# Kernel optimization log

Hardware: AMD Instinct MI355X
Metric: run time of the kernel (lower is better)

The kernel has to match this reference:

```python
import jax, jax.numpy as jnp
import numpy as np

NUM_HEADS = 8
D_MODEL = 512
HEAD_DIM = D_MODEL // NUM_HEADS


def _conv1x1(x, W, b):
    # Conv1d(kernel_size=1): x [B, Cin, N], W [Cout, Cin], b [Cout] -> [B, Cout, N]
    return jnp.einsum('oi,bin->bon', W, x) + b[None, :, None]


def setup_inputs() -> dict:
    key = jax.random.key(0)
    ks = jax.random.split(key, 12)
    B, D, N, Mlen = 4, D_MODEL, 2048, 2048
    inp = {
        'query': jax.random.normal(ks[0], (B, D, N), dtype=jnp.float32),
        'key':   jax.random.normal(ks[1], (B, D, Mlen), dtype=jnp.float32),
        'value': jax.random.normal(ks[2], (B, D, Mlen), dtype=jnp.float32),
        'M':     jnp.ones((B, N, Mlen), dtype=jnp.int32),
    }
    scale = 0.02
    inp['Wq'] = jax.random.normal(ks[3], (D, D), dtype=jnp.float32) * scale
    inp['bq'] = jnp.zeros((D,), dtype=jnp.float32)
    inp['Wk'] = jax.random.normal(ks[4], (D, D), dtype=jnp.float32) * scale
    inp['bk'] = jnp.zeros((D,), dtype=jnp.float32)
    inp['Wv'] = jax.random.normal(ks[5], (D, D), dtype=jnp.float32) * scale
    inp['bv'] = jnp.zeros((D,), dtype=jnp.float32)
    inp['Wm'] = jax.random.normal(ks[6], (D, D), dtype=jnp.float32) * scale
    inp['bm'] = jnp.zeros((D,), dtype=jnp.float32)
    return inp


def reference(query, key, value, M, Wq, bq, Wk, bk, Wv, bv, Wm, bm):
    B = query.shape[0]
    # 1x1-conv projections, then channel split as [head_dim, heads] (matches torch .view)
    q = _conv1x1(query, Wq, bq).reshape(B, HEAD_DIM, NUM_HEADS, -1)  # [B, d, h, N]
    k = _conv1x1(key,   Wk, bk).reshape(B, HEAD_DIM, NUM_HEADS, -1)  # [B, d, h, M]
    v = _conv1x1(value, Wv, bv).reshape(B, HEAD_DIM, NUM_HEADS, -1)  # [B, d, h, M]
    scores = jnp.einsum('bdhn,bdhm->bhnm', q, k) / jnp.sqrt(jnp.float32(HEAD_DIM))
    # mask: positions with M==0 are disallowed -> fill with -finfo.max
    bad = (1 - M)[:, None, :, :].astype(bool)  # [B, 1, N, M], broadcasts over heads
    scores = jnp.where(bad, -jnp.finfo(scores.dtype).max, scores)
    prob = jax.nn.softmax(scores, axis=-1)  # [B, h, N, M]
    x = jnp.einsum('bhnm,bdhm->bdhn', prob, v)  # [B, d, h, N]
    out = _conv1x1(x.reshape(B, HEAD_DIM * NUM_HEADS, -1), Wm, bm)  # [B, D, N]
    return out
```

## Files before the change

### kernel.cpp

```cpp
#include <hip/hip_runtime.h>

typedef __attribute__((ext_vector_type(8))) short s8v;
typedef __attribute__((ext_vector_type(4))) float f4v;
typedef unsigned short u16;
typedef unsigned long long u64;

#define DM 512
#define NH 8
#define HD 64
#define BB 4
#define NN 2048

__device__ __forceinline__ float bf2f(u16 x){ return __uint_as_float(((unsigned)x)<<16); }
__device__ __forceinline__ u16 f2bf(float f){
  unsigned u = __float_as_uint(f);
  u += 0x7FFFu + ((u>>16)&1u);
  return (u16)(u>>16);
}

__global__ void k_permute(const float* Wq, const float* bq, const float* Wk, const float* bk,
                          const float* Wv, const float* bv, const float* Wm,
                          u16* Wp, u16* Wmp, float* bp){
  int blk = blockIdx.x, tid = threadIdx.x;
  if (blk < 1536){
    int t = blk >> 9, op = blk & 511;
    int srow = ((op & 63) << 3) | (op >> 6);
    const float* W = (t==0) ? Wq : ((t==1) ? Wk : Wv);
    for (int j = tid; j < 512; j += 256)
      Wp[((size_t)t*512 + op)*512 + j] = f2bf(W[(size_t)srow*512 + j]);
  } else if (blk < 2048){
    int o = blk - 1536;
    for (int c = tid; c < 512; c += 256){
      int scol = ((c & 63) << 3) | (c >> 6);
      Wmp[(size_t)o*512 + c] = f2bf(Wm[(size_t)o*512 + scol]);
    }
  } else {
    for (int idx = tid; idx < 1536; idx += 256){
      int t = idx >> 9, op = idx & 511;
      const float* bs = (t==0) ? bq : ((t==1) ? bk : bv);
      int srow = ((op & 63) << 3) | (op >> 6);
      bp[idx] = bs[srow];
    }
  }
}

__global__ __launch_bounds__(256) void k_transpose(const float* q, const float* k, const float* v, u16* XT){
  __shared__ u16 T[64*72];
  int blk = blockIdx.x, tid = threadIdx.x;
  int rt = blk & 31; blk >>= 5;
  int it = blk & 7;  blk >>= 3;
  int b  = blk & 3;  int t = blk >> 2;
  const float* src = (t==0) ? q : ((t==1) ? k : v);
  src += (size_t)b*DM*NN;
  int i0 = it*64, r0 = rt*64;
  int il = tid>>4, rj = (tid&15)*4;
  #pragma unroll
  for (int p=0;p<4;p++){
    int i = il + p*16;
    float4 vv = *(const float4*)&src[(size_t)(i0+i)*NN + r0 + rj];
    float fv[4] = {vv.x, vv.y, vv.z, vv.w};
    #pragma unroll
    for (int qq=0;qq<4;qq++){
      int r = rj + qq;
      int sr = ((r&3)<<4) | (r>>2);
      T[sr*72 + i] = f2bf(fv[qq]);
    }
  }
  __syncthreads();
  u16* dst = XT + ((size_t)(t*4+b)*NN)*DM;
  int rl = tid>>3, ib = (tid&7)*8;
  #pragma unroll
  for (int p=0;p<2;p++){
    int r = rl + p*32;
    int sr = ((r&3)<<4) | (r>>2);
    s8v vv = *(s8v*)&T[sr*72 + ib];
    *(s8v*)&dst[(size_t)(r0+r)*DM + i0 + ib] = vv;
  }
}

__global__ __launch_bounds__(256) void k_proj(const u16* XT, const u16* Wp, const float* bp,
                                              u16* P, u16* VT){
  __shared__ u16 Xl[64*40];
  __shared__ u16 Wl[64*40];
  __shared__ u16 S[64*66];
  int blk = blockIdx.x, tid = threadIdx.x;
  int ot = blk & 7;  blk >>= 3;
  int rt = blk & 31; blk >>= 5;
  int b  = blk & 3;  int t = blk >> 2;
  int r0 = rt*64, o0 = ot*64;
  const u16* Xbase = XT + ((size_t)(t*4+b)*NN + r0)*DM;
  const u16* Wbase = Wp + ((size_t)t*512 + o0)*DM;
  int lr = tid>>2, lk = (tid&3)*8;
  int w = tid>>6, L = tid&63, li = L&15, lq = L>>4;
  f4v acc[4];
  #pragma unroll
  for (int j=0;j<4;j++) acc[j] = (f4v){0.f,0.f,0.f,0.f};
  for (int kk=0; kk<16; kk++){
    int k0 = kk*32;
    __syncthreads();
    *(s8v*)&Xl[lr*40+lk] = *(const s8v*)&Xbase[(size_t)lr*DM + k0 + lk];
    *(s8v*)&Wl[lr*40+lk] = *(const s8v*)&Wbase[(size_t)lr*DM + k0 + lk];
    __syncthreads();
    s8v a = *(s8v*)&Xl[(w*16+li)*40 + lq*8];
    #pragma unroll
    for (int j=0;j<4;j++){
      s8v bf = *(s8v*)&Wl[(j*16+li)*40 + lq*8];
      acc[j] = __builtin_amdgcn_mfma_f32_16x16x32_bf16(a, bf, acc[j], 0, 0, 0);
    }
  }
  int h = o0 >> 6;
  if (t < 2){
    float scale = (t==0) ? 0.125f : 1.0f;
    u16* Pb = P + (((size_t)(t*4+b)*NH + h)*NN)*HD;
    #pragma unroll
    for (int j=0;j<4;j++){
      int col = j*16 + li;
      float bias = bp[t*512 + o0 + col];
      #pragma unroll
      for (int ri=0; ri<4; ri++){
        int row = r0 + w*16 + lq*4 + ri;
        Pb[(size_t)row*HD + col] = f2bf((acc[j][ri] + bias)*scale);
      }
    }
  } else {
    #pragma unroll
    for (int j=0;j<4;j++){
      int col = j*16 + li;
      float bias = bp[2*512 + o0 + col];
      #pragma unroll
      for (int ri=0; ri<4; ri++){
        int rloc = w*16 + lq*4 + ri;
        S[rloc*66 + col] = f2bf(acc[j][ri] + bias);
      }
    }
    __syncthreads();
    int dl = tid>>2;
    u16* Vb = VT + (((size_t)b*NH + h)*HD)*NN;
    #pragma unroll
    for (int c=0;c<2;c++){
      int moff = (tid&3)*8 + c*32;
      s8v vv; u16* vp = (u16*)&vv;
      #pragma unroll
      for (int jj=0;jj<8;jj++) vp[jj] = S[(moff+jj)*66 + dl];
      *(s8v*)&Vb[(size_t)dl*NN + r0 + moff] = vv;
    }
  }
}

__global__ void k_maskpack(const int* M, u64* bits){
  int tid = threadIdx.x;
  size_t word = (size_t)blockIdx.x*4 + (tid>>6);
  int lane = tid & 63;
  int v = M[word*64 + lane];
  u64 bal = __ballot(v == 1);
  if (lane == 0) bits[word] = bal;
}

__global__ __launch_bounds__(256) void k_flash(const u16* P, const u16* VT, const u64* bits, u16* Xout){
  __shared__ u16 Ql[64*72];
  __shared__ u16 Kl[64*72];
  __shared__ u16 Vt[64*72];
  __shared__ u16 Pl[64*72];
  int blk = blockIdx.x, tid = threadIdx.x;
  int nt = blk & 31; int bh = blk >> 5;
  int b = bh >> 3, h = bh & 7;
  int n0 = nt*64;
  const size_t TSZ = (size_t)BB*NH*NN*HD;
  const u16* Qb = P + ((size_t)bh*NN + n0)*HD;
  const u16* Kb = P + TSZ + (size_t)bh*NN*HD;
  const u16* Vb = VT + (size_t)bh*HD*NN;

  int sm = tid>>3, sd = (tid&7)*8;
  int w = tid>>6, L = tid&63, li = L&15, lq = L>>4;
  int sli = ((li&3)<<2) | (li>>2);

  #pragma unroll
  for (int p=0;p<2;p++)
    *(s8v*)&Ql[(sm+p*32)*72 + sd] = *(const s8v*)&Qb[(size_t)(sm+p*32)*HD + sd];

  float ls[4];
  f4v O[4];
  #pragma unroll
  for (int ri=0;ri<4;ri++) ls[ri] = 0.f;
  #pragma unroll
  for (int j=0;j<4;j++) O[j] = (f4v){0.f,0.f,0.f,0.f};

  for (int mt=0; mt<32; mt++){
    int m0 = mt*64;
    s8v kreg[2], vreg[2];
    #pragma unroll
    for (int p=0;p<2;p++){
      kreg[p] = *(const s8v*)&Kb[(size_t)(m0+sm+p*32)*HD + sd];
      vreg[p] = *(const s8v*)&Vb[(size_t)(sm+p*32)*NN + m0 + sd];
    }
    u64 mw[4];
    #pragma unroll
    for (int ri=0;ri<4;ri++)
      mw[ri] = bits[((size_t)b*NN + n0 + w*16 + lq*4 + ri)*32 + mt];

    __syncthreads();
    #pragma unroll
    for (int p=0;p<2;p++){
      *(s8v*)&Kl[(sm+p*32)*72 + sd] = kreg[p];
      *(s8v*)&Vt[(sm+p*32)*72 + sd] = vreg[p];
    }
    __syncthreads();

    s8v a0 = *(s8v*)&Ql[(w*16+li)*72 + lq*8];
    s8v a1 = *(s8v*)&Ql[(w*16+li)*72 + 32 + lq*8];
    f4v S[4];
    #pragma unroll
    for (int j=0;j<4;j++){
      s8v b0 = *(s8v*)&Kl[(j*16+li)*72 + lq*8];
      s8v b1 = *(s8v*)&Kl[(j*16+li)*72 + 32 + lq*8];
      f4v c = (f4v){0.f,0.f,0.f,0.f};
      c = __builtin_amdgcn_mfma_f32_16x16x32_bf16(a0, b0, c, 0, 0, 0);
      c = __builtin_amdgcn_mfma_f32_16x16x32_bf16(a1, b1, c, 0, 0, 0);
      S[j] = c;
    }

    #pragma unroll
    for (int ri=0;ri<4;ri++){
      u64 wd = mw[ri];
      int srow = (w*16 + ((ri&3)<<2) + lq)*72;
      #pragma unroll
      for (int j=0;j<4;j++){
        float e = __expf(S[j][ri]);
        e = ((wd>>(j*16+li)) & 1ull) ? e : 0.f;
        ls[ri] += e;
        Pl[srow + j*16 + li] = f2bf(e);
      }
    }

    s8v ap0 = *(s8v*)&Pl[(w*16+sli)*72 + lq*8];
    s8v ap1 = *(s8v*)&Pl[(w*16+sli)*72 + 32 + lq*8];
    #pragma unroll
    for (int j2=0;j2<4;j2++){
      s8v b0 = *(s8v*)&Vt[(j2*16+li)*72 + lq*8];
      s8v b1 = *(s8v*)&Vt[(j2*16+li)*72 + 32 + lq*8];
      O[j2] = __builtin_amdgcn_mfma_f32_16x16x32_bf16(ap0, b0, O[j2], 0, 0, 0);
      O[j2] = __builtin_amdgcn_mfma_f32_16x16x32_bf16(ap1, b1, O[j2], 0, 0, 0);
    }
  }

  #pragma unroll
  for (int ri=0;ri<4;ri++){
    float r = ls[ri];
    r += __shfl_xor(r,1,16); r += __shfl_xor(r,2,16);
    r += __shfl_xor(r,4,16); r += __shfl_xor(r,8,16);
    ls[ri] = (r > 0.f) ? 1.0f/r : 0.f;
  }
  u16* Xo = Xout + ((size_t)b*NN)*DM + h*HD;
  #pragma unroll
  for (int j2=0;j2<4;j2++){
    int d = j2*16 + li;
    #pragma unroll
    for (int ri=0;ri<4;ri++){
      int n = n0 + w*16 + lq*4 + ri;
      Xo[(size_t)n*DM + d] = f2bf(O[j2][ri]*ls[ri]);
    }
  }
}

__global__ __launch_bounds__(256) void k_out(const u16* Wmp, const u16* Xout, const float* bm, float* out){
  __shared__ u16 Wl[64*40];
  __shared__ u16 Xl[64*40];
  int blk = blockIdx.x, tid = threadIdx.x;
  int nt = blk & 31; blk >>= 5;
  int ot = blk & 7;  int b = blk >> 3;
  int o0 = ot*64, n0 = nt*64;
  int lr = tid>>2, lk = (tid&3)*8;
  int w = tid>>6, L = tid&63, li = L&15, lq = L>>4;
  f4v acc[4];
  #pragma unroll
  for (int j=0;j<4;j++) acc[j] = (f4v){0.f,0.f,0.f,0.f};
  for (int kk=0; kk<16; kk++){
    int k0 = kk*32;
    __syncthreads();
    *(s8v*)&Wl[lr*40+lk] = *(const s8v*)&Wmp[(size_t)(o0+lr)*DM + k0 + lk];
    *(s8v*)&Xl[lr*40+lk] = *(const s8v*)&Xout[((size_t)b*NN + n0+lr)*DM + k0 + lk];
    __syncthreads();
    s8v a = *(s8v*)&Wl[(w*16+li)*40 + lq*8];
    #pragma unroll
    for (int j=0;j<4;j++){
      s8v bf = *(s8v*)&Xl[(j*16+li)*40 + lq*8];
      acc[j] = __builtin_amdgcn_mfma_f32_16x16x32_bf16(a, bf, acc[j], 0, 0, 0);
    }
  }
  #pragma unroll
  for (int j=0;j<4;j++){
    int n = n0 + j*16 + li;
    #pragma unroll
    for (int ri=0;ri<4;ri++){
      int o = o0 + w*16 + lq*4 + ri;
      out[((size_t)b*DM + o)*NN + n] = acc[j][ri] + bm[o];
    }
  }
}

extern "C" void kernel_launch(void* const* d_in, const int* in_sizes, int n_in,
                              void* d_out, int out_size, void* d_ws, size_t ws_size,
                              hipStream_t stream){
  const float* q  = (const float*)d_in[0];
  const float* k  = (const float*)d_in[1];
  const float* v  = (const float*)d_in[2];
  const int*   M  = (const int*)d_in[3];
  const float* Wq = (const float*)d_in[4];
  const float* bq = (const float*)d_in[5];
  const float* Wk = (const float*)d_in[6];
  const float* bk = (const float*)d_in[7];
  const float* Wv = (const float*)d_in[8];
  const float* bv = (const float*)d_in[9];
  const float* Wm = (const float*)d_in[10];
  const float* bm = (const float*)d_in[11];

  char* ws = (char*)d_ws;
  u16*   XT   = (u16*)(ws + 0);
  u16*   P    = (u16*)(ws + 25165824);
  u16*   VT   = (u16*)(ws + 41943040);
  u16*   Wp   = (u16*)(ws + 50331648);
  u16*   Wmp  = (u16*)(ws + 51904512);
  float* bp   = (float*)(ws + 52428800);
  u64*   bits = (u64*)(ws + 52434944);
  u16*   Xout = (u16*)(ws + 54532096);
  float* out  = (float*)d_out;

  k_permute<<<2049, 256, 0, stream>>>(Wq, bq, Wk, bk, Wv, bv, Wm, Wp, Wmp, bp);
  k_transpose<<<3072, 256, 0, stream>>>(q, k, v, XT);
  k_proj<<<3072, 256, 0, stream>>>(XT, Wp, bp, P, VT);
  k_maskpack<<<65536, 256, 0, stream>>>(M, bits);
  k_flash<<<1024, 256, 0, stream>>>(P, VT, bits, Xout);
  k_out<<<1024, 256, 0, stream>>>(Wmp, Xout, bm, out);
}
```

Before: 316.5 us.

## Use 128x128 GEMM tiles with direct-to-LDS loads, add mask-skip fast path and MFMA row sums

The projection and output GEMMs move from 64x64 to 128x128 block tiles with 4x4 MFMA accumulators per wave. Operands are loaded through global_load_lds into an XOR-swizzled LDS layout, which cuts block count and raises operand reuse. A new kernel ANDs mask bits per 64x64 tile so flash attention can skip per-row mask loads and selects when a tile is fully unmasked. Softmax row sums are now computed with an extra MFMA against a ones vector instead of shuffle reductions. This adds register pressure and an extra tiny kernel launch, and the row sums are now taken from bf16-rounded probabilities.

```diff
diff --git a/kernel.cpp b/kernel.cpp
--- a/kernel.cpp
+++ b/kernel.cpp
@@ -16,6 +16,10 @@
   unsigned u = __float_as_uint(f);
   u += 0x7FFFu + ((u>>16)&1u);
   return (u16)(u>>16);
+}
+__device__ __forceinline__ void gl2lds16(const u16* g, u16* l){
+  __builtin_amdgcn_global_load_lds((__attribute__((address_space(1))) void*)(g),
+                                   (__attribute__((address_space(3))) void*)(l), 16, 0, 0);
 }
 
 __global__ void k_permute(const float* Wq, const float* bq, const float* Wk, const float* bk,
@@ -80,69 +84,102 @@
 
 __global__ __launch_bounds__(256) void k_proj(const u16* XT, const u16* Wp, const float* bp,
                                               u16* P, u16* VT){
-  __shared__ u16 Xl[64*40];
-  __shared__ u16 Wl[64*40];
-  __shared__ u16 S[64*66];
+  __shared__ u16 Al[128*32];
+  __shared__ u16 Bl[128*32];
+  __shared__ u16 S[128*72];
   int blk = blockIdx.x, tid = threadIdx.x;
-  int ot = blk & 7;  blk >>= 3;
-  int rt = blk & 31; blk >>= 5;
-  int b  = blk & 3;  int t = blk >> 2;
-  int r0 = rt*64, o0 = ot*64;
-  const u16* Xbase = XT + ((size_t)(t*4+b)*NN + r0)*DM;
-  const u16* Wbase = Wp + ((size_t)t*512 + o0)*DM;
-  int lr = tid>>2, lk = (tid&3)*8;
+  int nt = blk & 3; int mt = blk >> 2;
+  int tb = mt >> 4;
+  int t  = tb >> 2, b = tb & 3;
+  int r0 = (mt & 15)*128, o0 = nt*128;
+  const u16* Abase = XT + ((size_t)tb*NN + r0)*DM;
+  const u16* Bbase = Wp + ((size_t)t*512 + o0)*DM;
+
   int w = tid>>6, L = tid&63, li = L&15, lq = L>>4;
-  f4v acc[4];
-  #pragma unroll
-  for (int j=0;j<4;j++) acc[j] = (f4v){0.f,0.f,0.f,0.f};
+  int wr = w>>1, wc = w&1;
+  int srow = tid>>2;
+  int g8   = ((tid&3) ^ ((tid>>3)&3))*8;
+  u16* AldsW = &Al[((tid&192))*8];
+  u16* BldsW = &Bl[((tid&192))*8];
+  int sw = (li>>1)&3;
+
+  f4v acc[4][4];
+  #pragma unroll
+  for (int a=0;a<4;a++)
+    #pragma unroll
+    for (int c2=0;c2<4;c2++) acc[a][c2] = (f4v){0.f,0.f,0.f,0.f};
+
   for (int kk=0; kk<16; kk++){
     int k0 = kk*32;
     __syncthreads();
-    *(s8v*)&Xl[lr*40+lk] = *(const s8v*)&Xbase[(size_t)lr*DM + k0 + lk];
-    *(s8v*)&Wl[lr*40+lk] = *(const s8v*)&Wbase[(size_t)lr*DM + k0 + lk];
-    __syncthreads();
-    s8v a = *(s8v*)&Xl[(w*16+li)*40 + lq*8];
-    #pragma unroll
-    for (int j=0;j<4;j++){
-      s8v bf = *(s8v*)&Wl[(j*16+li)*40 + lq*8];
-      acc[j] = __builtin_amdgcn_mfma_f32_16x16x32_bf16(a, bf, acc[j], 0, 0, 0);
-    }
-  }
-  int h = o0 >> 6;
+    #pragma unroll
+    for (int c=0;c<2;c++){
+      gl2lds16(&Abase[(size_t)(srow + c*64)*DM + k0 + g8], AldsW + c*2048);
+      gl2lds16(&Bbase[(size_t)(srow + c*64)*DM + k0 + g8], BldsW + c*2048);
+    }
+    __syncthreads();
+    s8v af[4], bfr[4];
+    #pragma unroll
+    for (int a=0;a<4;a++){
+      int r = wr*64 + a*16 + li;
+      af[a] = *(s8v*)&Al[r*32 + ((lq ^ sw))*8];
+    }
+    #pragma unroll
+    for (int c2=0;c2<4;c2++){
+      int r = wc*64 + c2*16 + li;
+      bfr[c2] = *(s8v*)&Bl[r*32 + ((lq ^ sw))*8];
+    }
+    #pragma unroll
+    for (int a=0;a<4;a++)
+      #pragma unroll
+      for (int c2=0;c2<4;c2++)
+        acc[a][c2] = __builtin_amdgcn_mfma_f32_16x16x32_bf16(af[a], bfr[c2], acc[a][c2], 0, 0, 0);
+  }
+
   if (t < 2){
     float scale = (t==0) ? 0.125f : 1.0f;
-    u16* Pb = P + (((size_t)(t*4+b)*NH + h)*NN)*HD;
-    #pragma unroll
-    for (int j=0;j<4;j++){
-      int col = j*16 + li;
+    #pragma unroll
+    for (int c2=0;c2<4;c2++){
+      int col = wc*64 + c2*16 + li;
+      int h = (o0 + col) >> 6, d = col & 63;
       float bias = bp[t*512 + o0 + col];
-      #pragma unroll
-      for (int ri=0; ri<4; ri++){
-        int row = r0 + w*16 + lq*4 + ri;
-        Pb[(size_t)row*HD + col] = f2bf((acc[j][ri] + bias)*scale);
+      u16* Pb = P + (((size_t)tb*NH + h)*NN)*HD + d;
+      #pragma unroll
+      for (int a=0;a<4;a++){
+        #pragma unroll
+        for (int ri=0;ri<4;ri++){
+          int row = r0 + wr*64 + a*16 + lq*4 + ri;
+          Pb[(size_t)row*HD] = f2bf((acc[a][c2][ri] + bias)*scale);
+        }
       }
     }
   } else {
     #pragma unroll
-    for (int j=0;j<4;j++){
-      int col = j*16 + li;
-      float bias = bp[2*512 + o0 + col];
-      #pragma unroll
-      for (int ri=0; ri<4; ri++){
-        int rloc = w*16 + lq*4 + ri;
-        S[rloc*66 + col] = f2bf(acc[j][ri] + bias);
+    for (int p=0;p<2;p++){
+      if (wc == p){
+        #pragma unroll
+        for (int c2=0;c2<4;c2++){
+          int cl = c2*16 + li;
+          float bias = bp[2*512 + o0 + p*64 + cl];
+          #pragma unroll
+          for (int a=0;a<4;a++)
+            #pragma unroll
+            for (int ri=0;ri<4;ri++)
+              S[(wr*64 + a*16 + lq*4 + ri)*72 + cl] = f2bf(acc[a][c2][ri] + bias);
+        }
       }
-    }
-    __syncthreads();
-    int dl = tid>>2;
-    u16* Vb = VT + (((size_t)b*NH + h)*HD)*NN;
-    #pragma unroll
-    for (int c=0;c<2;c++){
-      int moff = (tid&3)*8 + c*32;
-      s8v vv; u16* vp = (u16*)&vv;
-      #pragma unroll
-      for (int jj=0;jj<8;jj++) vp[jj] = S[(moff+jj)*66 + dl];
-      *(s8v*)&Vb[(size_t)dl*NN + r0 + moff] = vv;
+      __syncthreads();
+      int dl = tid & 63;
+      u16* Vb = VT + (((size_t)b*NH + (o0>>6) + p)*HD + dl)*NN + r0;
+      #pragma unroll
+      for (int it2=0; it2<4; it2++){
+        int mseg = (tid>>6) + it2*4;
+        s8v vv; u16* vp = (u16*)&vv;
+        #pragma unroll
+        for (int j=0;j<8;j++) vp[j] = S[(mseg*8+j)*72 + dl];
+        *(s8v*)&Vb[mseg*8] = vv;
+      }
+      __syncthreads();
     }
   }
 }
@@ -156,19 +193,39 @@
   if (lane == 0) bits[word] = bal;
 }
 
-__global__ __launch_bounds__(256) void k_flash(const u16* P, const u16* VT, const u64* bits, u16* Xout){
+__global__ __launch_bounds__(256) void k_maskand(const u64* bits, u64* allw){
+  __shared__ u64 red[256];
+  int bnt = blockIdx.x, tid = threadIdx.x;
+  int mt = tid & 31, rg = tid >> 5;
+  const u64* base = bits + (size_t)bnt*64*32;
+  u64 v = ~0ull;
+  #pragma unroll
+  for (int j=0;j<8;j++) v &= base[(size_t)(rg*8+j)*32 + mt];
+  red[tid] = v;
+  __syncthreads();
+  if (tid < 32){
+    u64 a = red[tid];
+    #pragma unroll
+    for (int g2=1; g2<8; g2++) a &= red[g2*32 + tid];
+    allw[(size_t)bnt*32 + tid] = a;
+  }
+}
+
+__global__ __launch_bounds__(256) void k_flash(const u16* P, const u16* VT, const u64* bits,
+                                               const u64* allw, u16* Xout){
   __shared__ u16 Ql[64*72];
   __shared__ u16 Kl[64*72];
   __shared__ u16 Vt[64*72];
   __shared__ u16 Pl[64*72];
   int blk = blockIdx.x, tid = threadIdx.x;
   int nt = blk & 31; int bh = blk >> 5;
-  int b = bh >> 3, h = bh & 7;
+  int b = bh >> 3;
   int n0 = nt*64;
   const size_t TSZ = (size_t)BB*NH*NN*HD;
   const u16* Qb = P + ((size_t)bh*NN + n0)*HD;
   const u16* Kb = P + TSZ + (size_t)bh*NN*HD;
   const u16* Vb = VT + (size_t)bh*HD*NN;
+  const u64* awp = allw + ((size_t)b*32 + nt)*32;
 
   int sm = tid>>3, sd = (tid&7)*8;
   int w = tid>>6, L = tid&63, li = L&15, lq = L>>4;
@@ -178,26 +235,25 @@
   for (int p=0;p<2;p++)
     *(s8v*)&Ql[(sm+p*32)*72 + sd] = *(const s8v*)&Qb[(size_t)(sm+p*32)*HD + sd];
 
-  float ls[4];
-  f4v O[4];
-  #pragma unroll
-  for (int ri=0;ri<4;ri++) ls[ri] = 0.f;
+  s8v ones;
+  #pragma unroll
+  for (int j=0;j<8;j++) ((u16*)&ones)[j] = 0x3F80;
+
+  f4v O[4], RS;
+  RS = (f4v){0.f,0.f,0.f,0.f};
   #pragma unroll
   for (int j=0;j<4;j++) O[j] = (f4v){0.f,0.f,0.f,0.f};
 
   for (int mt=0; mt<32; mt++){
     int m0 = mt*64;
+    u64 aw = awp[mt];
+    bool fast = (aw == ~0ull);
     s8v kreg[2], vreg[2];
     #pragma unroll
     for (int p=0;p<2;p++){
       kreg[p] = *(const s8v*)&Kb[(size_t)(m0+sm+p*32)*HD + sd];
       vreg[p] = *(const s8v*)&Vb[(size_t)(sm+p*32)*NN + m0 + sd];
     }
-    u64 mw[4];
-    #pragma unroll
-    for (int ri=0;ri<4;ri++)
-      mw[ri] = bits[((size_t)b*NN + n0 + w*16 + lq*4 + ri)*32 + mt];
-
     __syncthreads();
     #pragma unroll
     for (int p=0;p<2;p++){
@@ -219,21 +275,38 @@
       S[j] = c;
     }
 
-    #pragma unroll
-    for (int ri=0;ri<4;ri++){
-      u64 wd = mw[ri];
-      int srow = (w*16 + ((ri&3)<<2) + lq)*72;
-      #pragma unroll
-      for (int j=0;j<4;j++){
-        float e = __expf(S[j][ri]);
-        e = ((wd>>(j*16+li)) & 1ull) ? e : 0.f;
-        ls[ri] += e;
-        Pl[srow + j*16 + li] = f2bf(e);
+    if (fast){
+      #pragma unroll
+      for (int ri=0;ri<4;ri++){
+        int srow = (w*16 + ((ri&3)<<2) + lq)*72;
+        #pragma unroll
+        for (int j=0;j<4;j++){
+          unsigned u = __float_as_uint(__expf(S[j][ri])) + 0x8000u;
+          Pl[srow + j*16 + li] = (u16)(u>>16);
+        }
+      }
+    } else {
+      u64 mw[4];
+      #pragma unroll
+      for (int ri=0;ri<4;ri++)
+        mw[ri] = bits[((size_t)b*NN + n0 + w*16 + lq*4 + ri)*32 + mt];
+      #pragma unroll
+      for (int ri=0;ri<4;ri++){
+        int srow = (w*16 + ((ri&3)<<2) + lq)*72;
+        #pragma unroll
+        for (int j=0;j<4;j++){
+          float e = __expf(S[j][ri]);
+          e = ((mw[ri]>>(j*16+li)) & 1ull) ? e : 0.f;
+          unsigned u = __float_as_uint(e) + 0x8000u;
+          Pl[srow + j*16 + li] = (u16)(u>>16);
+        }
       }
     }
 
     s8v ap0 = *(s8v*)&Pl[(w*16+sli)*72 + lq*8];
     s8v ap1 = *(s8v*)&Pl[(w*16+sli)*72 + 32 + lq*8];
+    RS = __builtin_amdgcn_mfma_f32_16x16x32_bf16(ap0, ones, RS, 0, 0, 0);
+    RS = __builtin_amdgcn_mfma_f32_16x16x32_bf16(ap1, ones, RS, 0, 0, 0);
     #pragma unroll
     for (int j2=0;j2<4;j2++){
       s8v b0 = *(s8v*)&Vt[(j2*16+li)*72 + lq*8];
@@ -243,13 +316,10 @@
     }
   }
 
-  #pragma unroll
-  for (int ri=0;ri<4;ri++){
-    float r = ls[ri];
-    r += __shfl_xor(r,1,16); r += __shfl_xor(r,2,16);
-    r += __shfl_xor(r,4,16); r += __shfl_xor(r,8,16);
-    ls[ri] = (r > 0.f) ? 1.0f/r : 0.f;
-  }
+  float inv[4];
+  #pragma unroll
+  for (int ri=0;ri<4;ri++) inv[ri] = (RS[ri] > 0.f) ? 1.0f/RS[ri] : 0.f;
+  int h = bh & 7;
   u16* Xo = Xout + ((size_t)b*NN)*DM + h*HD;
   #pragma unroll
   for (int j2=0;j2<4;j2++){
@@ -257,43 +327,72 @@
     #pragma unroll
     for (int ri=0;ri<4;ri++){
       int n = n0 + w*16 + lq*4 + ri;
-      Xo[(size_t)n*DM + d] = f2bf(O[j2][ri]*ls[ri]);
+      Xo[(size_t)n*DM + d] = f2bf(O[j2][ri]*inv[ri]);
     }
   }
 }
 
 __global__ __launch_bounds__(256) void k_out(const u16* Wmp, const u16* Xout, const float* bm, float* out){
-  __shared__ u16 Wl[64*40];
-  __shared__ u16 Xl[64*40];
+  __shared__ u16 Al[128*32];
+  __shared__ u16 Bl[128*32];
   int blk = blockIdx.x, tid = threadIdx.x;
-  int nt = blk & 31; blk >>= 5;
-  int ot = blk & 7;  int b = blk >> 3;
-  int o0 = ot*64, n0 = nt*64;
-  int lr = tid>>2, lk = (tid&3)*8;
+  int nt = blk & 15; blk >>= 4;
+  int ot = blk & 3;  int b = blk >> 2;
+  int o0 = ot*128, n0 = nt*128;
+  const u16* Abase = Wmp + (size_t)o0*DM;
+  const u16* Bbase = Xout + ((size_t)b*NN + n0)*DM;
+
   int w = tid>>6, L = tid&63, li = L&15, lq = L>>4;
-  f4v acc[4];
-  #pragma unroll
-  for (int j=0;j<4;j++) acc[j] = (f4v){0.f,0.f,0.f,0.f};
+  int wr = w>>1, wc = w&1;
+  int srow = tid>>2;
+  int g8   = ((tid&3) ^ ((tid>>3)&3))*8;
+  u16* AldsW = &Al[((tid&192))*8];
+  u16* BldsW = &Bl[((tid&192))*8];
+  int sw = (li>>1)&3;
+
+  f4v acc[4][4];
+  #pragma unroll
+  for (int a=0;a<4;a++)
+    #pragma unroll
+    for (int c2=0;c2<4;c2++) acc[a][c2] = (f4v){0.f,0.f,0.f,0.f};
+
   for (int kk=0; kk<16; kk++){
     int k0 = kk*32;
     __syncthreads();
-    *(s8v*)&Wl[lr*40+lk] = *(const s8v*)&Wmp[(size_t)(o0+lr)*DM + k0 + lk];
-    *(s8v*)&Xl[lr*40+lk] = *(const s8v*)&Xout[((size_t)b*NN + n0+lr)*DM + k0 + lk];
-    __syncthreads();
-    s8v a = *(s8v*)&Wl[(w*16+li)*40 + lq*8];
-    #pragma unroll
-    for (int j=0;j<4;j++){
-      s8v bf = *(s8v*)&Xl[(j*16+li)*40 + lq*8];
-      acc[j] = __builtin_amdgcn_mfma_f32_16x16x32_bf16(a, bf, acc[j], 0, 0, 0);
-    }
-  }
-  #pragma unroll
-  for (int j=0;j<4;j++){
-    int n = n0 + j*16 + li;
+    #pragma unroll
+    for (int c=0;c<2;c++){
+      gl2lds16(&Abase[(size_t)(srow + c*64)*DM + k0 + g8], AldsW + c*2048);
+      gl2lds16(&Bbase[(size_t)(srow + c*64)*DM + k0 + g8], BldsW + c*2048);
+    }
+    __syncthreads();
+    s8v af[4], bfr[4];
+    #pragma unroll
+    for (int a=0;a<4;a++){
+      int r = wr*64 + a*16 + li;
+      af[a] = *(s8v*)&Al[r*32 + ((lq ^ sw))*8];
+    }
+    #pragma unroll
+    for (int c2=0;c2<4;c2++){
+      int r = wc*64 + c2*16 + li;
+      bfr[c2] = *(s8v*)&Bl[r*32 + ((lq ^ sw))*8];
+    }
+    #pragma unroll
+    for (int a=0;a<4;a++)
+      #pragma unroll
+      for (int c2=0;c2<4;c2++)
+        acc[a][c2] = __builtin_amdgcn_mfma_f32_16x16x32_bf16(af[a], bfr[c2], acc[a][c2], 0, 0, 0);
+  }
+
+  #pragma unroll
+  for (int a=0;a<4;a++){
     #pragma unroll
     for (int ri=0;ri<4;ri++){
-      int o = o0 + w*16 + lq*4 + ri;
-      out[((size_t)b*DM + o)*NN + n] = acc[j][ri] + bm[o];
+      int o = o0 + wr*64 + a*16 + lq*4 + ri;
+      float bias = bm[o];
+      float* ob = out + ((size_t)b*DM + o)*NN + n0 + wc*64;
+      #pragma unroll
+      for (int c2=0;c2<4;c2++)
+        ob[c2*16 + li] = acc[a][c2][ri] + bias;
     }
   }
 }
@@ -323,12 +422,14 @@
   float* bp   = (float*)(ws + 52428800);
   u64*   bits = (u64*)(ws + 52434944);
   u16*   Xout = (u16*)(ws + 54532096);
+  u64*   allw = (u64*)(ws + 62920704);
   float* out  = (float*)d_out;
 
   k_permute<<<2049, 256, 0, stream>>>(Wq, bq, Wk, bk, Wv, bv, Wm, Wp, Wmp, bp);
   k_transpose<<<3072, 256, 0, stream>>>(q, k, v, XT);
-  k_proj<<<3072, 256, 0, stream>>>(XT, Wp, bp, P, VT);
+  k_proj<<<768, 256, 0, stream>>>(XT, Wp, bp, P, VT);
   k_maskpack<<<65536, 256, 0, stream>>>(M, bits);
-  k_flash<<<1024, 256, 0, stream>>>(P, VT, bits, Xout);
-  k_out<<<1024, 256, 0, stream>>>(Wmp, Xout, bm, out);
-}
+  k_maskand<<<128, 256, 0, stream>>>(bits, allw);
+  k_flash<<<1024, 256, 0, stream>>>(P, VT, bits, allw, Xout);
+  k_out<<<256, 256, 0, stream>>>(Wmp, Xout, bm, out);
+}
```

After: 317.5 us. Within noise of the previous version (+0.3%).
